# Kernel optimization log

Measured on AMD Instinct MI355X. Metric: run time of the kernel, lower is better.

The kernel has to match this reference:

```python
import jax, jax.numpy as jnp
import numpy as np

B, S, D, H, DFF = 4, 2048, 1024, 16, 4096
DK = D // H
EPS = 1e-5


def setup_inputs() -> dict:
    key = jax.random.key(0)
    ks = jax.random.split(key, 8)
    s = 0.02
    return {
        "src": jax.random.normal(ks[0], (B, S, D), jnp.float32),
        "src_mask": jnp.ones((B, S, S), jnp.int32),
        "Wq": jax.random.normal(ks[1], (D, D), jnp.float32) * s,
        "Wk": jax.random.normal(ks[2], (D, D), jnp.float32) * s,
        "Wv": jax.random.normal(ks[3], (D, D), jnp.float32) * s,
        "Wo": jax.random.normal(ks[4], (D, D), jnp.float32) * s,
        "bo": jnp.zeros((D,), jnp.float32),
        "ln1_g": jnp.ones((D,), jnp.float32),
        "ln1_b": jnp.zeros((D,), jnp.float32),
        "W1": jax.random.normal(ks[5], (D, DFF), jnp.float32) * s,
        "b1": jnp.zeros((DFF,), jnp.float32),
        "W2": jax.random.normal(ks[6], (DFF, D), jnp.float32) * s,
        "b2": jnp.zeros((D,), jnp.float32),
        "ln2_g": jnp.ones((D,), jnp.float32),
        "ln2_b": jnp.zeros((D,), jnp.float32),
    }


def _layernorm(x, g, b):
    mu = jnp.mean(x, axis=-1, keepdims=True)
    var = jnp.mean(jnp.square(x - mu), axis=-1, keepdims=True)
    return (x - mu) * jax.lax.rsqrt(var + EPS) * g + b


def reference(src, src_mask, Wq, Wk, Wv, Wo, bo, ln1_g, ln1_b, W1, b1, W2, b2, ln2_g, ln2_b):
    scale = jnp.asarray(DK ** 0.5, src.dtype)
    # QKV projections: [B,S,D] -> [B,H,S,DK]
    def proj(x, W):
        return (x @ W).reshape(B, S, H, DK).transpose(0, 2, 1, 3)
    Q, K, V = proj(src, Wq), proj(src, Wk), proj(src, Wv)
    energy = jnp.einsum("bhqd,bhkd->bhqk", Q, K) / scale
    mask = src_mask[:, None, :, :]  # [B,1,S,S]
    energy = jnp.where(mask == 0, jnp.asarray(-1e30, energy.dtype), energy)
    attn = jax.nn.softmax(energy, axis=-1)
    out = jnp.einsum("bhqk,bhkd->bhqd", attn, V)  # [B,H,S,DK]
    out = out.transpose(0, 2, 1, 3).reshape(B, S, D)
    attn_out = out @ Wo + bo
    # residual + LayerNorm (dropout is identity in eval)
    x = _layernorm(src + attn_out, ln1_g, ln1_b)
    # position-wise FFN
    ff = jax.nn.relu(x @ W1 + b1) @ W2 + b2
    return _layernorm(x + ff, ln2_g, ln2_b)
```

## Files before the change

kernel.cpp:

```cpp
#include <hip/hip_runtime.h>

#define DEV static __device__ __forceinline__

typedef unsigned short u16;
typedef __attribute__((ext_vector_type(8))) short bf16x8;
typedef __attribute__((ext_vector_type(8))) unsigned short u16x8;
typedef __attribute__((ext_vector_type(4))) unsigned short u16x4;
typedef __attribute__((ext_vector_type(4))) float f32x4;

static constexpr int Bb = 4, Ss = 2048, Dd = 1024, Hh = 16, DFF = 4096;
static constexpr int BS = Bb * Ss;

DEV u16 f2bf(float f) {
  union { float f; unsigned u; } x; x.f = f;
  unsigned r = x.u + 0x7fffu + ((x.u >> 16) & 1u);
  return (u16)(r >> 16);
}

DEV void gload_lds16(const void* g, void* l) {
  __builtin_amdgcn_global_load_lds(
      (const __attribute__((address_space(1))) unsigned int*)g,
      (__attribute__((address_space(3))) unsigned int*)l, 16, 0, 0);
}

DEV unsigned lds_addr(const void* p) {
  return (unsigned)(size_t)(const __attribute__((address_space(3))) void*)p;
}

DEV f32x4 mfma16(bf16x8 a, bf16x8 b, f32x4 c) {
  return __builtin_amdgcn_mfma_f32_16x16x32_bf16(a, b, c, 0, 0, 0);
}

DEV bf16x8 cat8(u16x4 a, u16x4 b) {
  bf16x8 v;
#pragma unroll
  for (int j = 0; j < 4; j++) { v[j] = (short)a[j]; v[j + 4] = (short)b[j]; }
  return v;
}

#define TRRD(dst, addr, OFF)                                     \
  asm volatile("ds_read_b64_tr_b16 %0, %1 offset:" #OFF         \
               : "=v"(dst) : "v"(addr))

__global__ void cast_src_k(const float* __restrict__ in, u16* __restrict__ outp, int n) {
  int i = (blockIdx.x * 256 + threadIdx.x) * 4;
  const int stride = gridDim.x * 256 * 4;
  for (; i < n; i += stride) {
    float4 v = *(const float4*)(in + i);
    u16x4 o; o[0] = f2bf(v.x); o[1] = f2bf(v.y); o[2] = f2bf(v.z); o[3] = f2bf(v.w);
    *(u16x4*)(outp + i) = o;
  }
}

__global__ __launch_bounds__(256) void transpose_cast(const float* __restrict__ W,
                                                      u16* __restrict__ Wt, int K, int N) {
  __shared__ float t[32][33];
  const int n0 = blockIdx.x * 32, k0 = blockIdx.y * 32;
  const int tx = threadIdx.x & 31, ty = threadIdx.x >> 5;
#pragma unroll
  for (int i = 0; i < 4; i++) t[ty + i * 8][tx] = W[(size_t)(k0 + ty + i * 8) * N + n0 + tx];
  __syncthreads();
#pragma unroll
  for (int i = 0; i < 4; i++) Wt[(size_t)(n0 + ty + i * 8) * K + k0 + tx] = f2bf(t[tx][ty + i * 8]);
}

__global__ void mask_init_k(int* flags) { if (threadIdx.x < 4) flags[threadIdx.x] = 1; }
__global__ void mask_check_k(const int* __restrict__ mask, int* __restrict__ flags, int n) {
  int i = blockIdx.x * 256 + threadIdx.x;
  const int st = gridDim.x * 256;
  for (; i < n; i += st) if (mask[i] == 0) flags[i >> 22] = 0;
}

template <int MODE>
__global__ __launch_bounds__(256, 2) void gemm_bt(const u16* __restrict__ A,
                                                  const u16* __restrict__ Bt,
                                                  const float* __restrict__ bias,
                                                  void* __restrict__ C,
                                                  int M, int N, int K) {
  __shared__ alignas(16) u16 As[128 * 32];
  __shared__ alignas(16) u16 Bs[128 * 32];
  const int tid = threadIdx.x;
  const int lane = tid & 63;
  const int w = tid >> 6;
  const int wr = (w >> 1) * 64;
  const int wc = (w & 1) * 64;
  const int bm = blockIdx.y * 128;
  const int bn = blockIdx.x * 128;
  const int frow = lane & 15, fk = (lane >> 4) * 8;

  const int r0 = tid, r1 = 256 + tid;
  const u16* Ag0 = A + (size_t)(bm + (r0 >> 2)) * K + (r0 & 3) * 8;
  const u16* Ag1 = A + (size_t)(bm + (r1 >> 2)) * K + (r1 & 3) * 8;
  const u16* Bg0 = Bt + (size_t)(bn + (r0 >> 2)) * K + (r0 & 3) * 8;
  const u16* Bg1 = Bt + (size_t)(bn + (r1 >> 2)) * K + (r1 & 3) * 8;
  u16* As0 = As + (size_t)(w * 64) * 8;
  u16* As1 = As + (size_t)(256 + w * 64) * 8;
  u16* Bs0 = Bs + (size_t)(w * 64) * 8;
  u16* Bs1 = Bs + (size_t)(256 + w * 64) * 8;

  f32x4 acc[4][4] = {};

  for (int k0 = 0; k0 < K; k0 += 32) {
    gload_lds16(Ag0 + k0, As0);
    gload_lds16(Ag1 + k0, As1);
    gload_lds16(Bg0 + k0, Bs0);
    gload_lds16(Bg1 + k0, Bs1);
    __syncthreads();
    bf16x8 af[4], bfr[4];
#pragma unroll
    for (int m = 0; m < 4; m++) af[m] = *(const bf16x8*)&As[(wr + m * 16 + frow) * 32 + fk];
#pragma unroll
    for (int n = 0; n < 4; n++) bfr[n] = *(const bf16x8*)&Bs[(wc + n * 16 + frow) * 32 + fk];
#pragma unroll
    for (int m = 0; m < 4; m++)
#pragma unroll
      for (int n = 0; n < 4; n++)
        acc[m][n] = mfma16(af[m], bfr[n], acc[m][n]);
    __syncthreads();
  }

#pragma unroll
  for (int m = 0; m < 4; m++) {
#pragma unroll
    for (int n = 0; n < 4; n++) {
      const int col = bn + wc + n * 16 + frow;
      const float bv = (MODE == 2) ? bias[col] : 0.f;
      const float sc = (MODE == 3 && col < Dd) ? 0.125f : 1.f;
#pragma unroll
      for (int r = 0; r < 4; r++) {
        const int row = bm + wr + m * 16 + (lane >> 4) * 4 + r;
        float v = acc[m][n][r];
        if (MODE == 2) v = fmaxf(v + bv, 0.f);
        if (MODE == 3) v *= sc;
        if (MODE == 0) ((float*)C)[(size_t)row * N + col] = v;
        else           ((u16*)C)[(size_t)row * N + col] = f2bf(v);
      }
    }
  }
}

template <int MODE>
__global__ __launch_bounds__(512, 2) void gemm8p(const u16* __restrict__ A,
                                                 const u16* __restrict__ Bt,
                                                 const float* __restrict__ bias,
                                                 void* __restrict__ C,
                                                 int M, int N, int K) {
  __shared__ alignas(128) u16 lds[65536];
  const int tid = threadIdx.x, lane = tid & 63, w = tid >> 6;
  const int wm = w >> 2, wc = w & 3;
  const int frow = lane & 15, hi = lane >> 4;
  const int bm = blockIdx.y * 256, bn = blockIdx.x * 256;
  const int NT = K >> 6;

  const int cs = ((tid & 7) ^ ((tid >> 3) & 7)) * 8;
  const int sr = w * 8 + ((lane >> 3) & 7);
  const u16* Ab = A + (size_t)(bm + sr) * K + cs;
  const u16* Bbp = Bt + (size_t)(bn + sr) * K + cs;
  u16* lw = lds + w * 512;

  const int c0 = (hi * 8) ^ ((frow & 7) << 3);
  const u16* Abase = lds + wm * 8192 + frow * 64;
  const u16* Bbase = lds + 32768 + (wc >> 1) * 8192 + (wc & 1) * 4096 + frow * 64;

  f32x4 acc[8][4] = {};
  bf16x8 af0[4][2], af1[4][2], bf0[2][2], bf1[2][2];

#define STG(Pb, hh, kk, reg)                                                     \
  do {                                                                           \
    gload_lds16((Pb) + (size_t)((hh) * 128) * K + (kk), lw + (reg));             \
    gload_lds16((Pb) + (size_t)((hh) * 128 + 64) * K + (kk), lw + (reg) + 4096); \
  } while (0)
#define LDA(dst, sb, mh)                                                              \
  do {                                                                                \
    _Pragma("unroll") for (int m = 0; m < 4; m++) {                                   \
      dst[m][0] = *(const bf16x8*)(Abase + (sb) + ((mh) * 4 + m) * 1024 + c0);        \
      dst[m][1] = *(const bf16x8*)(Abase + (sb) + ((mh) * 4 + m) * 1024 + (c0 ^ 32)); \
    }                                                                                 \
  } while (0)
#define LDB(dst, sb, nh)                                                              \
  do {                                                                                \
    _Pragma("unroll") for (int n = 0; n < 2; n++) {                                   \
      dst[n][0] = *(const bf16x8*)(Bbase + (sb) + ((nh) * 2 + n) * 1024 + c0);        \
      dst[n][1] = *(const bf16x8*)(Bbase + (sb) + ((nh) * 2 + n) * 1024 + (c0 ^ 32)); \
    }                                                                                 \
  } while (0)
#define MM(AF, BF, mh, nh)                                                             \
  do {                                                                                 \
    __builtin_amdgcn_s_setprio(1);                                                     \
    _Pragma("unroll") for (int m = 0; m < 4; m++) _Pragma("unroll") for (int n = 0;    \
                                                                        n < 2; n++) { \
      acc[(mh)*4+m][(nh)*2+n] = mfma16(AF[m][0], BF[n][0], acc[(mh)*4+m][(nh)*2+n]);   \
      acc[(mh)*4+m][(nh)*2+n] = mfma16(AF[m][1], BF[n][1], acc[(mh)*4+m][(nh)*2+n]);   \
    }                                                                                  \
    __builtin_amdgcn_s_setprio(0);                                                     \
  } while (0)
#define BAR asm volatile("s_barrier" ::: "memory")
#define VMC(n) asm volatile("s_waitcnt vmcnt(" #n ")" ::: "memory")

  STG(Ab, 0, 0, 0);        STG(Ab, 1, 0, 8192);
  STG(Bbp, 0, 0, 32768);   STG(Bbp, 1, 0, 40960);
  STG(Ab, 0, 64, 16384);   STG(Ab, 1, 64, 24576);
  VMC(0);
  BAR;

  const int NI = NT >> 1;
#pragma unroll 1
  for (int i = 0; i < NI; ++i) {
    const int T = i * 2;
    const int kT1 = (T + 1) << 6;
    const int kT2 = (T + 2 < NT ? T + 2 : NT - 1) << 6;
    const int kT3 = (T + 3 < NT ? T + 3 : NT - 1) << 6;
    LDA(af0, 0, 0); LDB(bf0, 0, 0);
    STG(Bbp, 0, kT1, 49152);
    BAR; MM(af0, bf0, 0, 0); BAR;
    LDA(af1, 0, 1);
    STG(Bbp, 1, kT1, 57344);
    BAR; MM(af1, bf0, 1, 0); BAR;
    LDB(bf1, 0, 1);
    STG(Ab, 0, kT2, 0);
    BAR; MM(af0, bf1, 0, 1); BAR;
    STG(Ab, 1, kT2, 8192);
    VMC(4); BAR; MM(af1, bf1, 1, 1); BAR;
    LDA(af0, 16384, 0); LDB(bf0, 16384, 0);
    STG(Bbp, 0, kT2, 32768);
    BAR; MM(af0, bf0, 0, 0); BAR;
    LDA(af1, 16384, 1);
    STG(Bbp, 1, kT2, 40960);
    BAR; MM(af1, bf0, 1, 0); BAR;
    LDB(bf1, 16384, 1);
    STG(Ab, 0, kT3, 16384);
    BAR; MM(af0, bf1, 0, 1); BAR;
    STG(Ab, 1, kT3, 24576);
    VMC(4); BAR; MM(af1, bf1, 1, 1); BAR;
  }

#undef STG
#undef LDA
#undef LDB
#undef MM
#undef BAR
#undef VMC

#pragma unroll
  for (int m = 0; m < 8; m++) {
#pragma unroll
    for (int n = 0; n < 4; n++) {
      const int col = bn + wc * 64 + n * 16 + frow;
      const float bv = (MODE == 2) ? bias[col] : 0.f;
      const float sc = (MODE == 3 && col < Dd) ? 0.125f : 1.f;
#pragma unroll
      for (int r = 0; r < 4; r++) {
        const int row = bm + wm * 128 + m * 16 + hi * 4 + r;
        float v = acc[m][n][r];
        if (MODE == 2) v = fmaxf(v + bv, 0.f);
        if (MODE == 3) v *= sc;
        if (MODE == 0) ((float*)C)[(size_t)row * N + col] = v;
        else           ((u16*)C)[(size_t)row * N + col] = f2bf(v);
      }
    }
  }
}

__global__ __launch_bounds__(256, 3) void attn_fwd(const u16* __restrict__ qkv,
                                                   const int* __restrict__ mask,
                                                   const int* __restrict__ mflag,
                                                   u16* __restrict__ outb) {
  __shared__ alignas(128) u16 Ks[2 * 4096];
  __shared__ alignas(128) u16 Vs[2 * 4096];
  __shared__ alignas(16)  u16 Pl[4 * 16 * 72];

  const int bx = blockIdx.x;
  const int qt = bx & 31;
  const int h = (bx >> 5) & 15;
  const int b = bx >> 9;
  const int tid = threadIdx.x;
  const int lane = tid & 63;
  const int w = tid >> 6;
  const int frow = lane & 15, hi = lane >> 4;
  const int qbase = qt * 64 + w * 16;

  bf16x8 qf[2];
  {
    const u16* qp = qkv + (size_t)(b * Ss + qbase + frow) * 3072 + h * 64 + hi * 8;
    qf[0] = *(const bf16x8*)(qp);
    qf[1] = *(const bf16x8*)(qp + 32);
  }
  const int allones = mflag[b];
  u16* Plw = Pl + w * (16 * 72);

  f32x4 oacc[4] = {};
  float mrow = -1e30f, lrow = 0.f;

  const size_t kvb = (size_t)(b * Ss) * 3072 + 1024 + h * 64;
  const int kcol_s = tid >> 2;
  const int dsw = ((tid & 3) ^ (kcol_s & 3)) * 8;
  const u16* Kg0 = qkv + kvb + (size_t)kcol_s * 3072 + dsw;
  const u16* Kg1 = Kg0 + 32;
  int kV0, dkV0, kV1, dkV1;
  {
    int p = tid, T = p >> 3, j = (p >> 1) & 3, hh = p & 1;
    kV0 = ((T >> 3) & 1) * 32 + (T & 3) * 8 + ((T >> 2) & 1) * 4 + j;
    dkV0 = ((T >> 4) & 3) * 16 + hh * 8;
    p = tid + 256; T = p >> 3; j = (p >> 1) & 3; hh = p & 1;
    kV1 = ((T >> 3) & 1) * 32 + (T & 3) * 8 + ((T >> 2) & 1) * 4 + j;
    dkV1 = ((T >> 4) & 3) * 16 + hh * 8;
  }
  const u16* Vg0 = qkv + kvb + 1024 + (size_t)kV0 * 3072 + dkV0;
  const u16* Vg1 = qkv + kvb + 1024 + (size_t)kV1 * 3072 + dkV1;

  const unsigned vbase = lds_addr(Vs) + lane * 8;

  gload_lds16(Kg0, Ks + w * 512);
  gload_lds16(Kg1, Ks + 2048 + w * 512);
  gload_lds16(Vg0, Vs + w * 512);
  gload_lds16(Vg1, Vs + 2048 + w * 512);
  __syncthreads();

#pragma unroll 1
  for (int kt = 0; kt < 32; kt++) {
    const int cur = kt & 1;
    if (kt < 31) {
      const size_t soff = (size_t)(kt + 1) * 64 * 3072;
      u16* Kb = Ks + (cur ^ 1) * 4096;
      u16* Vb = Vs + (cur ^ 1) * 4096;
      gload_lds16(Kg0 + soff, Kb + w * 512);
      gload_lds16(Kg1 + soff, Kb + 2048 + w * 512);
      gload_lds16(Vg0 + soff, Vb + w * 512);
      gload_lds16(Vg1 + soff, Vb + 2048 + w * 512);
    }
    const u16* Kbuf = Ks + cur * 4096;

    f32x4 sacc[4] = {};
    const int kswz = (hi ^ (frow & 3)) * 8;
#pragma unroll
    for (int ks = 0; ks < 2; ks++)
#pragma unroll
      for (int n = 0; n < 4; n++) {
        bf16x8 kf = *(const bf16x8*)&Kbuf[ks * 2048 + (n * 16 + frow) * 32 + kswz];
        sacc[n] = mfma16(kf, qf[ks], sacc[n]);
      }

    const int srow = kt * 64;
    float sv[16];
#pragma unroll
    for (int n = 0; n < 4; n++)
#pragma unroll
      for (int r = 0; r < 4; r++) {
        float s = sacc[n][r];
        if (!allones) {
          const int qq = b * Ss + qbase + frow;
          const int kk = srow + n * 16 + hi * 4 + r;
          if (mask[(size_t)qq * Ss + kk] == 0) s = -1e30f;
        }
        sv[n * 4 + r] = s;
      }
    float mt = sv[0];
#pragma unroll
    for (int i = 1; i < 16; i++) mt = fmaxf(mt, sv[i]);
    mt = fmaxf(mt, __shfl_xor(mt, 16));
    mt = fmaxf(mt, __shfl_xor(mt, 32));
    const float mn = fmaxf(mrow, mt);
    const float al = __expf(mrow - mn);
    mrow = mn;
    float ps[16], rs = 0.f;
#pragma unroll
    for (int i = 0; i < 16; i++) { ps[i] = __expf(sv[i] - mn); rs += ps[i]; }
    rs += __shfl_xor(rs, 16);
    rs += __shfl_xor(rs, 32);
    lrow = lrow * al + rs;
    float alr[4];
#pragma unroll
    for (int r = 0; r < 4; r++) alr[r] = __shfl(al, (lane & 48) | (hi * 4 + r));
#pragma unroll
    for (int n = 0; n < 4; n++) {
      oacc[n][0] *= alr[0]; oacc[n][1] *= alr[1];
      oacc[n][2] *= alr[2]; oacc[n][3] *= alr[3];
    }
#pragma unroll
    for (int n = 0; n < 4; n++)
#pragma unroll
      for (int r = 0; r < 4; r++)
        Plw[frow * 72 + n * 16 + hi * 4 + r] = f2bf(ps[n * 4 + r]);

    const unsigned vaddr = vbase + (cur << 13);
    u16x4 t0, t1, t2, t3, t4, t5, t6, t7;
    TRRD(t0, vaddr, 0);    TRRD(t1, vaddr, 512);
    TRRD(t2, vaddr, 2048); TRRD(t3, vaddr, 2560);
    TRRD(t4, vaddr, 4096); TRRD(t5, vaddr, 4608);
    TRRD(t6, vaddr, 6144); TRRD(t7, vaddr, 6656);
    {
      bf16x8 pa = *(const bf16x8*)&Plw[frow * 72 + hi * 8];
      asm volatile("s_waitcnt lgkmcnt(0)" ::: "memory");
      __builtin_amdgcn_sched_barrier(0);
      oacc[0] = mfma16(pa, cat8(t0, t1), oacc[0]);
      oacc[1] = mfma16(pa, cat8(t2, t3), oacc[1]);
      oacc[2] = mfma16(pa, cat8(t4, t5), oacc[2]);
      oacc[3] = mfma16(pa, cat8(t6, t7), oacc[3]);
    }
    TRRD(t0, vaddr, 1024); TRRD(t1, vaddr, 1536);
    TRRD(t2, vaddr, 3072); TRRD(t3, vaddr, 3584);
    TRRD(t4, vaddr, 5120); TRRD(t5, vaddr, 5632);
    TRRD(t6, vaddr, 7168); TRRD(t7, vaddr, 7680);
    {
      bf16x8 pa = *(const bf16x8*)&Plw[frow * 72 + 32 + hi * 8];
      asm volatile("s_waitcnt lgkmcnt(0)" ::: "memory");
      __builtin_amdgcn_sched_barrier(0);
      oacc[0] = mfma16(pa, cat8(t0, t1), oacc[0]);
      oacc[1] = mfma16(pa, cat8(t2, t3), oacc[1]);
      oacc[2] = mfma16(pa, cat8(t4, t5), oacc[2]);
      oacc[3] = mfma16(pa, cat8(t6, t7), oacc[3]);
    }
    __syncthreads();
  }

  float lr[4];
#pragma unroll
  for (int r = 0; r < 4; r++) lr[r] = __shfl(lrow, (lane & 48) | (hi * 4 + r));
#pragma unroll
  for (int n = 0; n < 4; n++)
#pragma unroll
    for (int r = 0; r < 4; r++) {
      const int q = qbase + hi * 4 + r;
      const int dk = n * 16 + frow;
      outb[(size_t)(b * Ss + q) * 1024 + h * 64 + dk] = f2bf(oacc[n][r] / lr[r]);
    }
}

__global__ __launch_bounds__(256) void ln_fuse(const float* __restrict__ a,
                                               const float* __restrict__ c,
                                               const float* __restrict__ bias,
                                               const float* __restrict__ g,
                                               const float* __restrict__ be,
                                               float* __restrict__ of,
                                               u16* __restrict__ ob) {
  __shared__ float red[4];
  const int tid = threadIdx.x;
  const size_t base = (size_t)blockIdx.x * 1024 + tid * 4;
  float4 va = *(const float4*)(a + base);
  float4 vc = *(const float4*)(c + base);
  float4 vb = *(const float4*)(bias + tid * 4);
  const float s0 = va.x + vc.x + vb.x, s1 = va.y + vc.y + vb.y;
  const float s2 = va.z + vc.z + vb.z, s3 = va.w + vc.w + vb.w;
  float sum = s0 + s1 + s2 + s3;
#pragma unroll
  for (int o = 32; o; o >>= 1) sum += __shfl_xor(sum, o);
  if ((tid & 63) == 0) red[tid >> 6] = sum;
  __syncthreads();
  const float mu = (red[0] + red[1] + red[2] + red[3]) * (1.f / 1024.f);
  __syncthreads();
  const float d0 = s0 - mu, d1 = s1 - mu, d2 = s2 - mu, d3 = s3 - mu;
  float vs = d0 * d0 + d1 * d1 + d2 * d2 + d3 * d3;
#pragma unroll
  for (int o = 32; o; o >>= 1) vs += __shfl_xor(vs, o);
  if ((tid & 63) == 0) red[tid >> 6] = vs;
  __syncthreads();
  const float var = (red[0] + red[1] + red[2] + red[3]) * (1.f / 1024.f);
  const float rs = rsqrtf(var + 1e-5f);
  float4 vg = *(const float4*)(g + tid * 4);
  float4 ve = *(const float4*)(be + tid * 4);
  const float y0 = d0 * rs * vg.x + ve.x, y1 = d1 * rs * vg.y + ve.y;
  const float y2 = d2 * rs * vg.z + ve.z, y3 = d3 * rs * vg.w + ve.w;
  if (of) { float4 y; y.x = y0; y.y = y1; y.z = y2; y.w = y3; *(float4*)(of + base) = y; }
  if (ob) { u16x4 o; o[0] = f2bf(y0); o[1] = f2bf(y1); o[2] = f2bf(y2); o[3] = f2bf(y3);
            *(u16x4*)(ob + base) = o; }
}

extern "C" void kernel_launch(void* const* d_in, const int* in_sizes, int n_in,
                              void* d_out, int out_size, void* d_ws, size_t ws_size,
                              hipStream_t stream) {
  const float* src = (const float*)d_in[0];
  const int* mask = (const int*)d_in[1];
  const float* Wq = (const float*)d_in[2];
  const float* Wk = (const float*)d_in[3];
  const float* Wv = (const float*)d_in[4];
  const float* Wo = (const float*)d_in[5];
  const float* bo = (const float*)d_in[6];
  const float* g1 = (const float*)d_in[7];
  const float* be1 = (const float*)d_in[8];
  const float* W1 = (const float*)d_in[9];
  const float* b1 = (const float*)d_in[10];
  const float* W2 = (const float*)d_in[11];
  const float* b2 = (const float*)d_in[12];
  const float* g2 = (const float*)d_in[13];
  const float* be2 = (const float*)d_in[14];
  float* outp = (float*)d_out;
  (void)in_sizes; (void)n_in; (void)out_size; (void)ws_size;

  char* ws = (char*)d_ws;
  size_t off = 0;
  auto take = [&](size_t bytes) -> char* {
    char* p = ws + off;
    off = (off + bytes + 255) & ~(size_t)255;
    return p;
  };
  u16* srcb  = (u16*)take((size_t)BS * Dd * 2);
  u16* wqkvt = (u16*)take((size_t)3 * Dd * Dd * 2);
  u16* wot   = (u16*)take((size_t)Dd * Dd * 2);
  u16* w1t   = (u16*)take((size_t)Dd * DFF * 2);
  u16* w2t   = (u16*)take((size_t)DFF * Dd * 2);
  char* qkvr = take((size_t)BS * 3 * Dd * 2);
  u16* qkvb  = (u16*)qkvr;
  float* Cf  = (float*)qkvr;
  u16* attnb = (u16*)take((size_t)BS * Dd * 2);
  float* xf  = (float*)take((size_t)BS * Dd * 4);
  u16* hb    = (u16*)take((size_t)BS * DFF * 2);
  int* flags = (int*)take(256);

  cast_src_k<<<2048, 256, 0, stream>>>(src, srcb, BS * Dd);
  transpose_cast<<<dim3(32, 32), 256, 0, stream>>>(Wq, wqkvt,                Dd, Dd);
  transpose_cast<<<dim3(32, 32), 256, 0, stream>>>(Wk, wqkvt + Dd * Dd,      Dd, Dd);
  transpose_cast<<<dim3(32, 32), 256, 0, stream>>>(Wv, wqkvt + 2 * Dd * Dd,  Dd, Dd);
  transpose_cast<<<dim3(32, 32), 256, 0, stream>>>(Wo, wot, Dd, Dd);
  transpose_cast<<<dim3(128, 32), 256, 0, stream>>>(W1, w1t, Dd, DFF);
  transpose_cast<<<dim3(32, 128), 256, 0, stream>>>(W2, w2t, DFF, Dd);
  mask_init_k<<<1, 64, 0, stream>>>(flags);
  mask_check_k<<<2048, 256, 0, stream>>>(mask, flags, Bb * Ss * Ss);

  gemm8p<3><<<dim3(3 * Dd / 256, BS / 256), 512, 0, stream>>>(srcb, wqkvt, nullptr, qkvb,
                                                              BS, 3 * Dd, Dd);
  attn_fwd<<<Bb * Hh * (Ss / 64), 256, 0, stream>>>(qkvb, mask, flags, attnb);
  gemm_bt<0><<<dim3(Dd / 128, BS / 128), 256, 0, stream>>>(attnb, wot, nullptr, Cf,
                                                           BS, Dd, Dd);
  ln_fuse<<<BS, 256, 0, stream>>>(src, Cf, bo, g1, be1, xf, attnb);
  gemm8p<2><<<dim3(DFF / 256, BS / 256), 512, 0, stream>>>(attnb, w1t, b1, hb,
                                                           BS, DFF, Dd);
  gemm_bt<0><<<dim3(Dd / 128, BS / 128), 256, 0, stream>>>(hb, w2t, nullptr, Cf,
                                                           BS, Dd, DFF);
  ln_fuse<<<BS, 256, 0, stream>>>(xf, Cf, b2, g2, be2, outp, nullptr);
}
```

Baseline: 667.3 us.

## Add 128x256 pipelined GEMM, exp2 softmax with lazy rescale, packed bf16 converts

Adds gemm8ph, a 128x256-tile, 8-wave pipelined MFMA GEMM with swizzled LDS and double-buffered global-to-LDS loads. It replaces the simple gemm_bt kernel for the Wo and W2 projections and gemm8p for the QKV projection, giving those narrow-N GEMMs more blocks and better pipelining. Attention now folds log2(e) into the Q scale so it can use exp2f, and only rescales the running max and output accumulators when the max grows by more than 8. P is converted to bf16 with packed v_cvt_pk_bf16_f32 instructions. The lazy rescale lets probabilities exceed 1 (up to 2^8 before a rescale), which adds some bf16 precision risk.

```diff
diff --git a/kernel.cpp b/kernel.cpp
--- a/kernel.cpp
+++ b/kernel.cpp
@@ -10,11 +10,18 @@
 
 static constexpr int Bb = 4, Ss = 2048, Dd = 1024, Hh = 16, DFF = 4096;
 static constexpr int BS = Bb * Ss;
+#define QSCALE 0.18033688011112042f
 
 DEV u16 f2bf(float f) {
   union { float f; unsigned u; } x; x.f = f;
   unsigned r = x.u + 0x7fffu + ((x.u >> 16) & 1u);
   return (u16)(r >> 16);
+}
+
+DEV unsigned cvtpk(float lo, float hi) {
+  unsigned r;
+  asm("v_cvt_pk_bf16_f32 %0, %1, %2" : "=v"(r) : "v"(lo), "v"(hi));
+  return r;
 }
 
 DEV void gload_lds16(const void* g, void* l) {
@@ -69,74 +76,6 @@
   int i = blockIdx.x * 256 + threadIdx.x;
   const int st = gridDim.x * 256;
   for (; i < n; i += st) if (mask[i] == 0) flags[i >> 22] = 0;
-}
-
-template <int MODE>
-__global__ __launch_bounds__(256, 2) void gemm_bt(const u16* __restrict__ A,
-                                                  const u16* __restrict__ Bt,
-                                                  const float* __restrict__ bias,
-                                                  void* __restrict__ C,
-                                                  int M, int N, int K) {
-  __shared__ alignas(16) u16 As[128 * 32];
-  __shared__ alignas(16) u16 Bs[128 * 32];
-  const int tid = threadIdx.x;
-  const int lane = tid & 63;
-  const int w = tid >> 6;
-  const int wr = (w >> 1) * 64;
-  const int wc = (w & 1) * 64;
-  const int bm = blockIdx.y * 128;
-  const int bn = blockIdx.x * 128;
-  const int frow = lane & 15, fk = (lane >> 4) * 8;
-
-  const int r0 = tid, r1 = 256 + tid;
-  const u16* Ag0 = A + (size_t)(bm + (r0 >> 2)) * K + (r0 & 3) * 8;
-  const u16* Ag1 = A + (size_t)(bm + (r1 >> 2)) * K + (r1 & 3) * 8;
-  const u16* Bg0 = Bt + (size_t)(bn + (r0 >> 2)) * K + (r0 & 3) * 8;
-  const u16* Bg1 = Bt + (size_t)(bn + (r1 >> 2)) * K + (r1 & 3) * 8;
-  u16* As0 = As + (size_t)(w * 64) * 8;
-  u16* As1 = As + (size_t)(256 + w * 64) * 8;
-  u16* Bs0 = Bs + (size_t)(w * 64) * 8;
-  u16* Bs1 = Bs + (size_t)(256 + w * 64) * 8;
-
-  f32x4 acc[4][4] = {};
-
-  for (int k0 = 0; k0 < K; k0 += 32) {
-    gload_lds16(Ag0 + k0, As0);
-    gload_lds16(Ag1 + k0, As1);
-    gload_lds16(Bg0 + k0, Bs0);
-    gload_lds16(Bg1 + k0, Bs1);
-    __syncthreads();
-    bf16x8 af[4], bfr[4];
-#pragma unroll
-    for (int m = 0; m < 4; m++) af[m] = *(const bf16x8*)&As[(wr + m * 16 + frow) * 32 + fk];
-#pragma unroll
-    for (int n = 0; n < 4; n++) bfr[n] = *(const bf16x8*)&Bs[(wc + n * 16 + frow) * 32 + fk];
-#pragma unroll
-    for (int m = 0; m < 4; m++)
-#pragma unroll
-      for (int n = 0; n < 4; n++)
-        acc[m][n] = mfma16(af[m], bfr[n], acc[m][n]);
-    __syncthreads();
-  }
-
-#pragma unroll
-  for (int m = 0; m < 4; m++) {
-#pragma unroll
-    for (int n = 0; n < 4; n++) {
-      const int col = bn + wc + n * 16 + frow;
-      const float bv = (MODE == 2) ? bias[col] : 0.f;
-      const float sc = (MODE == 3 && col < Dd) ? 0.125f : 1.f;
-#pragma unroll
-      for (int r = 0; r < 4; r++) {
-        const int row = bm + wr + m * 16 + (lane >> 4) * 4 + r;
-        float v = acc[m][n][r];
-        if (MODE == 2) v = fmaxf(v + bv, 0.f);
-        if (MODE == 3) v *= sc;
-        if (MODE == 0) ((float*)C)[(size_t)row * N + col] = v;
-        else           ((u16*)C)[(size_t)row * N + col] = f2bf(v);
-      }
-    }
-  }
 }
 
 template <int MODE>
@@ -247,10 +186,138 @@
     for (int n = 0; n < 4; n++) {
       const int col = bn + wc * 64 + n * 16 + frow;
       const float bv = (MODE == 2) ? bias[col] : 0.f;
-      const float sc = (MODE == 3 && col < Dd) ? 0.125f : 1.f;
+      const float sc = (MODE == 3 && col < Dd) ? QSCALE : 1.f;
 #pragma unroll
       for (int r = 0; r < 4; r++) {
         const int row = bm + wm * 128 + m * 16 + hi * 4 + r;
+        float v = acc[m][n][r];
+        if (MODE == 2) v = fmaxf(v + bv, 0.f);
+        if (MODE == 3) v *= sc;
+        if (MODE == 0) ((float*)C)[(size_t)row * N + col] = v;
+        else           ((u16*)C)[(size_t)row * N + col] = f2bf(v);
+      }
+    }
+  }
+}
+
+template <int MODE>
+__global__ __launch_bounds__(512, 2) void gemm8ph(const u16* __restrict__ A,
+                                                  const u16* __restrict__ Bt,
+                                                  const float* __restrict__ bias,
+                                                  void* __restrict__ C,
+                                                  int M, int N, int K) {
+  __shared__ alignas(128) u16 lds[49152];
+  const int tid = threadIdx.x, lane = tid & 63, w = tid >> 6;
+  const int wm = w >> 2, wc = w & 3;
+  const int frow = lane & 15, hi = lane >> 4;
+  const int bm = blockIdx.y * 128, bn = blockIdx.x * 256;
+  const int NT = K >> 6;
+
+  const int cs = ((tid & 7) ^ ((tid >> 3) & 7)) * 8;
+  const int sr = w * 8 + ((lane >> 3) & 7);
+  const u16* Ab = A + (size_t)(bm + sr) * K + cs;
+  const u16* Bbp = Bt + (size_t)(bn + sr) * K + cs;
+  u16* lwA = lds + w * 512;
+  u16* lwB = lds + 16384 + w * 512;
+
+  const int c0 = (hi * 8) ^ ((frow & 7) << 3);
+  const u16* Abase = lds + wm * 4096 + frow * 64;
+  const u16* Bbase = lds + 16384 + wc * 4096 + frow * 64;
+
+  f32x4 acc[4][4] = {};
+  bf16x8 af0[2][2], af1[2][2], bf0[2][2], bf1[2][2];
+
+#define STGA(kk, reg)                                              \
+  do {                                                             \
+    gload_lds16(Ab + (kk), lwA + (reg));                           \
+    gload_lds16(Ab + (size_t)64 * K + (kk), lwA + (reg) + 4096);   \
+  } while (0)
+#define STGB(hh, kk, reg)                                                            \
+  do {                                                                               \
+    gload_lds16(Bbp + (size_t)((hh) * 128) * K + (kk), lwB + (reg) + (hh) * 8192);   \
+    gload_lds16(Bbp + (size_t)((hh) * 128 + 64) * K + (kk),                          \
+                lwB + (reg) + (hh) * 8192 + 4096);                                   \
+  } while (0)
+#define LDA2(dst, sb, mh)                                                             \
+  do {                                                                                \
+    _Pragma("unroll") for (int m = 0; m < 2; m++) {                                   \
+      dst[m][0] = *(const bf16x8*)(Abase + (sb) + ((mh) * 2 + m) * 1024 + c0);        \
+      dst[m][1] = *(const bf16x8*)(Abase + (sb) + ((mh) * 2 + m) * 1024 + (c0 ^ 32)); \
+    }                                                                                 \
+  } while (0)
+#define LDB2(dst, sb, nh)                                                             \
+  do {                                                                                \
+    _Pragma("unroll") for (int n = 0; n < 2; n++) {                                   \
+      dst[n][0] = *(const bf16x8*)(Bbase + (sb) + ((nh) * 2 + n) * 1024 + c0);        \
+      dst[n][1] = *(const bf16x8*)(Bbase + (sb) + ((nh) * 2 + n) * 1024 + (c0 ^ 32)); \
+    }                                                                                 \
+  } while (0)
+#define MM2(AF, BF, mh, nh)                                                            \
+  do {                                                                                 \
+    __builtin_amdgcn_s_setprio(1);                                                     \
+    _Pragma("unroll") for (int m = 0; m < 2; m++) _Pragma("unroll") for (int n = 0;    \
+                                                                        n < 2; n++) { \
+      acc[(mh)*2+m][(nh)*2+n] = mfma16(AF[m][0], BF[n][0], acc[(mh)*2+m][(nh)*2+n]);   \
+      acc[(mh)*2+m][(nh)*2+n] = mfma16(AF[m][1], BF[n][1], acc[(mh)*2+m][(nh)*2+n]);   \
+    }                                                                                  \
+    __builtin_amdgcn_s_setprio(0);                                                     \
+  } while (0)
+#define BAR asm volatile("s_barrier" ::: "memory")
+#define VMC(n) asm volatile("s_waitcnt vmcnt(" #n ")" ::: "memory")
+
+  STGA(0, 0);
+  STGB(0, 0, 0); STGB(1, 0, 0);
+  STGA(64, 8192);
+  VMC(0);
+  BAR;
+
+  const int NI = NT >> 1;
+#pragma unroll 1
+  for (int i = 0; i < NI; ++i) {
+    const int T = i * 2;
+    const int kT1 = (T + 1) << 6;
+    const int kT2 = (T + 2 < NT ? T + 2 : NT - 1) << 6;
+    const int kT3 = (T + 3 < NT ? T + 3 : NT - 1) << 6;
+    LDA2(af0, 0, 0); LDB2(bf0, 0, 0);
+    STGB(0, kT1, 16384);
+    BAR; MM2(af0, bf0, 0, 0); BAR;
+    LDA2(af1, 0, 1);
+    STGB(1, kT1, 16384);
+    BAR; MM2(af1, bf0, 1, 0); BAR;
+    LDB2(bf1, 0, 1);
+    STGA(kT2, 0);
+    BAR; MM2(af0, bf1, 0, 1); BAR;
+    VMC(2); BAR; MM2(af1, bf1, 1, 1); BAR;
+    LDA2(af0, 8192, 0); LDB2(bf0, 16384, 0);
+    STGB(0, kT2, 0);
+    BAR; MM2(af0, bf0, 0, 0); BAR;
+    LDA2(af1, 8192, 1);
+    STGB(1, kT2, 0);
+    BAR; MM2(af1, bf0, 1, 0); BAR;
+    LDB2(bf1, 16384, 1);
+    STGA(kT3, 8192);
+    BAR; MM2(af0, bf1, 0, 1); BAR;
+    VMC(2); BAR; MM2(af1, bf1, 1, 1); BAR;
+  }
+
+#undef STGA
+#undef STGB
+#undef LDA2
+#undef LDB2
+#undef MM2
+#undef BAR
+#undef VMC
+
+#pragma unroll
+  for (int m = 0; m < 4; m++) {
+#pragma unroll
+    for (int n = 0; n < 4; n++) {
+      const int col = bn + wc * 64 + n * 16 + frow;
+      const float bv = (MODE == 2) ? bias[col] : 0.f;
+      const float sc = (MODE == 3 && col < Dd) ? QSCALE : 1.f;
+#pragma unroll
+      for (int r = 0; r < 4; r++) {
+        const int row = bm + wm * 64 + m * 16 + hi * 4 + r;
         float v = acc[m][n][r];
         if (MODE == 2) v = fmaxf(v + bv, 0.f);
         if (MODE == 3) v *= sc;
@@ -359,28 +426,31 @@
     for (int i = 1; i < 16; i++) mt = fmaxf(mt, sv[i]);
     mt = fmaxf(mt, __shfl_xor(mt, 16));
     mt = fmaxf(mt, __shfl_xor(mt, 32));
-    const float mn = fmaxf(mrow, mt);
-    const float al = __expf(mrow - mn);
-    mrow = mn;
+    if (__any(mt > mrow + 8.f)) {
+      const float mn = fmaxf(mrow, mt);
+      const float al = exp2f(mrow - mn);
+      mrow = mn;
+      lrow *= al;
+      float alr[4];
+#pragma unroll
+      for (int r = 0; r < 4; r++) alr[r] = __shfl(al, (lane & 48) | (hi * 4 + r));
+#pragma unroll
+      for (int n = 0; n < 4; n++) {
+        oacc[n][0] *= alr[0]; oacc[n][1] *= alr[1];
+        oacc[n][2] *= alr[2]; oacc[n][3] *= alr[3];
+      }
+    }
     float ps[16], rs = 0.f;
 #pragma unroll
-    for (int i = 0; i < 16; i++) { ps[i] = __expf(sv[i] - mn); rs += ps[i]; }
+    for (int i = 0; i < 16; i++) { ps[i] = exp2f(sv[i] - mrow); rs += ps[i]; }
     rs += __shfl_xor(rs, 16);
     rs += __shfl_xor(rs, 32);
-    lrow = lrow * al + rs;
-    float alr[4];
-#pragma unroll
-    for (int r = 0; r < 4; r++) alr[r] = __shfl(al, (lane & 48) | (hi * 4 + r));
+    lrow += rs;
 #pragma unroll
     for (int n = 0; n < 4; n++) {
-      oacc[n][0] *= alr[0]; oacc[n][1] *= alr[1];
-      oacc[n][2] *= alr[2]; oacc[n][3] *= alr[3];
-    }
-#pragma unroll
-    for (int n = 0; n < 4; n++)
-#pragma unroll
-      for (int r = 0; r < 4; r++)
-        Plw[frow * 72 + n * 16 + hi * 4 + r] = f2bf(ps[n * 4 + r]);
+      *(unsigned*)(Plw + frow * 72 + n * 16 + hi * 4)     = cvtpk(ps[n * 4 + 0], ps[n * 4 + 1]);
+      *(unsigned*)(Plw + frow * 72 + n * 16 + hi * 4 + 2) = cvtpk(ps[n * 4 + 2], ps[n * 4 + 3]);
+    }
 
     const unsigned vaddr = vbase + (cur << 13);
     u16x4 t0, t1, t2, t3, t4, t5, t6, t7;
@@ -516,15 +586,15 @@
   mask_init_k<<<1, 64, 0, stream>>>(flags);
   mask_check_k<<<2048, 256, 0, stream>>>(mask, flags, Bb * Ss * Ss);
 
-  gemm8p<3><<<dim3(3 * Dd / 256, BS / 256), 512, 0, stream>>>(srcb, wqkvt, nullptr, qkvb,
-                                                              BS, 3 * Dd, Dd);
+  gemm8ph<3><<<dim3(3 * Dd / 256, BS / 128), 512, 0, stream>>>(srcb, wqkvt, nullptr, qkvb,
+                                                               BS, 3 * Dd, Dd);
   attn_fwd<<<Bb * Hh * (Ss / 64), 256, 0, stream>>>(qkvb, mask, flags, attnb);
-  gemm_bt<0><<<dim3(Dd / 128, BS / 128), 256, 0, stream>>>(attnb, wot, nullptr, Cf,
+  gemm8ph<0><<<dim3(Dd / 256, BS / 128), 512, 0, stream>>>(attnb, wot, nullptr, Cf,
                                                            BS, Dd, Dd);
   ln_fuse<<<BS, 256, 0, stream>>>(src, Cf, bo, g1, be1, xf, attnb);
   gemm8p<2><<<dim3(DFF / 256, BS / 256), 512, 0, stream>>>(attnb, w1t, b1, hb,
                                                            BS, DFF, Dd);
-  gemm_bt<0><<<dim3(Dd / 128, BS / 128), 256, 0, stream>>>(hb, w2t, nullptr, Cf,
+  gemm8ph<0><<<dim3(Dd / 256, BS / 128), 512, 0, stream>>>(hb, w2t, nullptr, Cf,
                                                            BS, Dd, DFF);
   ln_fuse<<<BS, 256, 0, stream>>>(xf, Cf, b2, g2, be2, outp, nullptr);
 }
```

After: 670.8 us. About the same (+0.5%).
